# Optimization experiments

Measured on AMD Instinct MI355X. Metric: run time of the kernel, lower is better.

Reference implementation:

```python
import jax, jax.numpy as jnp
import numpy as np

SEQ = 2048
HID = 1024
NH = 16
HD = HID // NH


def setup_inputs() -> dict:
    key = jax.random.key(0)
    ks = jax.random.split(key, 5)
    s = 0.02
    return {
        "hidden_states": jax.random.normal(ks[0], (SEQ, HID), dtype=jnp.float32),
        "w_attn": jax.random.normal(ks[1], (HID, 3 * HID), dtype=jnp.float32) * s,
        "b_attn": jax.random.normal(ks[2], (3 * HID,), dtype=jnp.float32) * s,
        "w_proj": jax.random.normal(ks[3], (HID, HID), dtype=jnp.float32) * s,
        "b_proj": jax.random.normal(ks[4], (HID,), dtype=jnp.float32) * s,
    }


def reference(hidden_states, w_attn, b_attn, w_proj, b_proj):
    S = hidden_states.shape[0]
    qkv = hidden_states @ w_attn + b_attn          # [S, 3H]
    q, k, v = jnp.split(qkv, 3, axis=-1)
    q = q.reshape(S, NH, HD)
    k = k.reshape(S, NH, HD)
    v = v.reshape(S, NH, HD)
    sm_scale = 1.0 / np.sqrt(HD).astype(np.float32)
    # explicit scores [h, q, k] in fp32, as in the torch module
    scores = jnp.einsum('qhd,khd->hqk', q.astype(jnp.float32), k.astype(jnp.float32))
    scores = scores * sm_scale
    causal = jnp.tril(jnp.ones((S, S), dtype=bool))  # [q, k]
    scores = jnp.where(causal[None, :, :], scores, -jnp.inf)
    probs = jax.nn.softmax(scores, axis=-1)
    attn = jnp.einsum('hqk,khd->qhd', probs, v.astype(jnp.float32))  # [S, NH, HD]
    attn = attn.reshape(S, HID).astype(hidden_states.dtype)
    return attn @ w_proj + b_proj
```

## Files before the change

### kernel.cpp

```cpp
#include <hip/hip_runtime.h>
#include <cstdint>
#include <cstddef>

#define SEQ 2048
#define HID 1024
#define NHEAD 16
#define HDIM 64

typedef _Float16 f16;
typedef f16 half8 __attribute__((ext_vector_type(8)));
typedef f16 half4 __attribute__((ext_vector_type(4)));
typedef f16 half2_ __attribute__((ext_vector_type(2)));
typedef float f32x4 __attribute__((ext_vector_type(4)));

#define ASYNC_COPY16(g, l)                                                    \
  __builtin_amdgcn_global_load_lds(                                           \
      (const __attribute__((address_space(1))) void*)(const void*)(g),        \
      (__attribute__((address_space(3))) void*)(void*)(l), 16, 0, 0)

__global__ __launch_bounds__(256) void prologue(
    const float* __restrict__ h, const float* __restrict__ wa,
    const float* __restrict__ wp, f16* __restrict__ h16,
    f16* __restrict__ waT, f16* __restrict__ wpT) {
  const int b = blockIdx.x, tid = threadIdx.x;
  if (b >= 4096) {
    int i = ((b - 4096) * 256 + tid) * 4;
    float4 v = *(const float4*)(h + i);
    half4 o;
    o[0] = (f16)v.x; o[1] = (f16)v.y; o[2] = (f16)v.z; o[3] = (f16)v.w;
    *(half4*)(h16 + i) = o;
    return;
  }
  const float* src; f16* dst; int C, bx, by;
  if (b < 3072) { src = wa; dst = waT; C = 3072; bx = b % 96; by = b / 96; }
  else { int t = b - 3072; src = wp; dst = wpT; C = 1024; bx = t & 31; by = t >> 5; }
  __shared__ float tile[32][33];
  const int tx = tid & 31, ty = tid >> 5;
  const int c0 = bx * 32, r0 = by * 32;
#pragma unroll
  for (int i = 0; i < 32; i += 8)
    tile[ty + i][tx] = src[(size_t)(r0 + ty + i) * C + c0 + tx];
  __syncthreads();
#pragma unroll
  for (int i = 0; i < 32; i += 8)
    dst[(size_t)(c0 + ty + i) * 1024 + r0 + tx] = (f16)tile[tx][ty + i];
}

template <int BM, int BN, bool OUT16>
__global__ __launch_bounds__(256) void gemm_f16(
    const f16* __restrict__ A, const f16* __restrict__ Bt,
    const float* __restrict__ bias, void* __restrict__ Cout, int M, int N,
    int K) {
  constexpr int FM = BM / 32, FN = BN / 32;
  __shared__ __align__(16) f16 sA[BM * 32];
  __shared__ __align__(16) f16 sB[BN * 32];
  const int tid = threadIdx.x;
  const int wave = tid >> 6, lane = tid & 63;
  const int quad = lane >> 4, l16 = lane & 15;
  const int m0 = blockIdx.y * BM, n0 = blockIdx.x * BN;
  const int wm = (wave >> 1) * (BM / 2), wn = (wave & 1) * (BN / 2);
  const int rowA = lane >> 2, chunkA = lane & 3;

  f32x4 acc[FM][FN] = {};

  for (int k0 = 0; k0 < K; k0 += 32) {
#pragma unroll
    for (int r = wave; r < BM / 16; r += 4)
      ASYNC_COPY16(A + (size_t)(m0 + r * 16 + rowA) * K + k0 + chunkA * 8,
                   &sA[r * 512]);
#pragma unroll
    for (int r = wave; r < BN / 16; r += 4)
      ASYNC_COPY16(Bt + (size_t)(n0 + r * 16 + rowA) * K + k0 + chunkA * 8,
                   &sB[r * 512]);
    __syncthreads();

    half8 af[FM], bf[FN];
#pragma unroll
    for (int i = 0; i < FM; i++)
      af[i] = *(const half8*)&sA[(wm + i * 16 + l16) * 32 + quad * 8];
#pragma unroll
    for (int j = 0; j < FN; j++)
      bf[j] = *(const half8*)&sB[(wn + j * 16 + l16) * 32 + quad * 8];
#pragma unroll
    for (int i = 0; i < FM; i++)
#pragma unroll
      for (int j = 0; j < FN; j++)
        acc[i][j] = __builtin_amdgcn_mfma_f32_16x16x32_f16(af[i], bf[j],
                                                           acc[i][j], 0, 0, 0);
    __syncthreads();
  }

#pragma unroll
  for (int i = 0; i < FM; i++) {
    int row = m0 + wm + i * 16 + quad * 4;
#pragma unroll
    for (int j = 0; j < FN; j++) {
      int col = n0 + wn + j * 16 + l16;
      float bv = bias[col];
#pragma unroll
      for (int r = 0; r < 4; r++) {
        float v = acc[i][j][r] + bv;
        if (OUT16)
          ((f16*)Cout)[(size_t)(row + r) * N + col] = (f16)v;
        else
          ((float*)Cout)[(size_t)(row + r) * N + col] = v;
      }
    }
  }
}

#define LROW 72
__global__ __launch_bounds__(256, 3) void attn_split(
    const f16* __restrict__ qkv, f16* __restrict__ out,
    f16* __restrict__ Opart, float* __restrict__ ml) {
  const int b = blockIdx.x;
  const int h = b / 40;
  const int t = b % 40;
  int m, c, nc;
  if (t < 4)       { m = t;                 c = 0;      nc = 1; }
  else if (t < 12) { int u = t - 4;  m = 4 + (u >> 1);  c = u & 1; nc = 2; }
  else if (t < 24) { int u = t - 12; m = 8 + u / 3;     c = u % 3; nc = 3; }
  else             { int u = t - 24; m = 12 + (u >> 2); c = u & 3; nc = 4; }
  const int q0 = m * 128;
  const int T = 2 * m + 2;
  const int kt0 = c * 8;
  const int kt1 = (kt0 + 8 < T) ? kt0 + 8 : T;
  const int maskFrom = 2 * m;

  __shared__ __align__(16) f16 sK[64 * LROW];
  __shared__ __align__(16) f16 sVt[64 * LROW];
  __shared__ __align__(16) f16 sP[4][32 * LROW];

  const int tid = threadIdx.x;
  const int wave = tid >> 6, lane = tid & 63;
  const int quad = lane >> 4, l16 = lane & 15;

  const f16 qs = (f16)0.18033688f;
  half8 qf[2][2];
#pragma unroll
  for (int g = 0; g < 2; g++) {
    const f16* qb = qkv + (size_t)(q0 + wave * 32 + g * 16 + l16) * 3072 +
                    h * HDIM + quad * 8;
    qf[g][0] = *(const half8*)qb;
    qf[g][1] = *(const half8*)(qb + 32);
#pragma unroll
    for (int j = 0; j < 8; j++) { qf[g][0][j] *= qs; qf[g][1][j] *= qs; }
  }

  const f16* kbase = qkv + HID + h * HDIM;
  const f16* vbase = qkv + 2 * HID + h * HDIM;
  const int ks_row = tid >> 3, ks_cc = tid & 7;
  const int vs_d = tid & 63, vs_g = tid >> 6;

  f32x4 o[2][4] = {};
  float m_i[2] = {-1e30f, -1e30f}, l_i[2] = {0.f, 0.f};
  half8 kreg[2], vreg[2];

  auto prefetch = [&](int kt) {
    const int k0 = kt * 64;
#pragma unroll
    for (int i = 0; i < 2; i++) {
      kreg[i] = *(const half8*)(kbase + (size_t)(k0 + ks_row + i * 32) * 3072 +
                                ks_cc * 8);
      half8 col;
#pragma unroll
      for (int j = 0; j < 8; j++)
        col[j] = vbase[(size_t)(k0 + (vs_g + i * 4) * 8 + j) * 3072 + vs_d];
      vreg[i] = col;
    }
  };

  prefetch(kt0);
  for (int kt = kt0; kt < kt1; kt++) {
    const int k0 = kt * 64;
#pragma unroll
    for (int i = 0; i < 2; i++) {
      *(half8*)&sK[(ks_row + i * 32) * LROW + ks_cc * 8] = kreg[i];
      *(half8*)&sVt[vs_d * LROW + (vs_g + i * 4) * 8] = vreg[i];
    }
    __syncthreads();
    if (kt + 1 < kt1) prefetch(kt + 1);

    f32x4 sacc[2][4] = {};
#pragma unroll
    for (int kb = 0; kb < 4; kb++) {
      half8 kf0 = *(const half8*)&sK[(kb * 16 + l16) * LROW + quad * 8];
      half8 kf1 = *(const half8*)&sK[(kb * 16 + l16) * LROW + 32 + quad * 8];
#pragma unroll
      for (int g = 0; g < 2; g++) {
        sacc[g][kb] = __builtin_amdgcn_mfma_f32_16x16x32_f16(kf0, qf[g][0],
                                                             sacc[g][kb], 0, 0, 0);
        sacc[g][kb] = __builtin_amdgcn_mfma_f32_16x16x32_f16(kf1, qf[g][1],
                                                             sacc[g][kb], 0, 0, 0);
      }
    }
    if (kt >= maskFrom) {
#pragma unroll
      for (int g = 0; g < 2; g++) {
        const int qg = q0 + wave * 32 + g * 16 + l16;
#pragma unroll
        for (int kb = 0; kb < 4; kb++) {
          int kg = k0 + kb * 16 + quad * 4;
#pragma unroll
          for (int r = 0; r < 4; r++)
            if (kg + r > qg) sacc[g][kb][r] = -1e30f;
        }
      }
    }
#pragma unroll
    for (int g = 0; g < 2; g++) {
      float mx = -1e30f;
#pragma unroll
      for (int kb = 0; kb < 4; kb++)
#pragma unroll
        for (int r = 0; r < 4; r++) mx = fmaxf(mx, sacc[g][kb][r]);
      mx = fmaxf(mx, __shfl_xor(mx, 16));
      mx = fmaxf(mx, __shfl_xor(mx, 32));
      const float mnew = fmaxf(m_i[g], mx);
      const float alpha = exp2f(m_i[g] - mnew);
      float rs = 0.f;
#pragma unroll
      for (int kb = 0; kb < 4; kb++)
#pragma unroll
        for (int r = 0; r < 4; r++) {
          float p = exp2f(sacc[g][kb][r] - mnew);
          sacc[g][kb][r] = p;
          rs += p;
        }
      rs += __shfl_xor(rs, 16);
      rs += __shfl_xor(rs, 32);
      l_i[g] = l_i[g] * alpha + rs;
      m_i[g] = mnew;
#pragma unroll
      for (int j = 0; j < 4; j++)
#pragma unroll
        for (int r = 0; r < 4; r++) o[g][j][r] *= alpha;
      f16* pw = &sP[wave][(g * 16 + l16) * LROW];
#pragma unroll
      for (int kb = 0; kb < 4; kb++)
#pragma unroll
        for (int rp = 0; rp < 2; rp++) {
          half2_ pv;
          pv[0] = (f16)sacc[g][kb][rp * 2];
          pv[1] = (f16)sacc[g][kb][rp * 2 + 1];
          *(half2_*)&pw[kb * 16 + quad * 4 + rp * 2] = pv;
        }
    }
#pragma unroll
    for (int j = 0; j < 4; j++) {
      half8 vf0 = *(const half8*)&sVt[(j * 16 + l16) * LROW + quad * 8];
      half8 vf1 = *(const half8*)&sVt[(j * 16 + l16) * LROW + 32 + quad * 8];
#pragma unroll
      for (int g = 0; g < 2; g++) {
        half8 pf0 = *(const half8*)&sP[wave][(g * 16 + l16) * LROW + quad * 8];
        half8 pf1 =
            *(const half8*)&sP[wave][(g * 16 + l16) * LROW + 32 + quad * 8];
        o[g][j] = __builtin_amdgcn_mfma_f32_16x16x32_f16(vf0, pf0, o[g][j], 0, 0, 0);
        o[g][j] = __builtin_amdgcn_mfma_f32_16x16x32_f16(vf1, pf1, o[g][j], 0, 0, 0);
      }
    }
    __syncthreads();
  }

  if (nc == 1) {
#pragma unroll
    for (int g = 0; g < 2; g++) {
      const float inv = 1.f / l_i[g];
      f16* orow =
          out + (size_t)(q0 + wave * 32 + g * 16 + l16) * HID + h * HDIM;
#pragma unroll
      for (int j = 0; j < 4; j++) {
        half4 hv;
#pragma unroll
        for (int r = 0; r < 4; r++) hv[r] = (f16)(o[g][j][r] * inv);
        *(half4*)&orow[j * 16 + quad * 4] = hv;
      }
    }
  } else {
    int base;
    if (m < 8)       base = (m - 4) * 2;
    else if (m < 12) base = 8 + (m - 8) * 3;
    else             base = 20 + (m - 12) * 4;
    const int slot = h * 36 + base + c;
#pragma unroll
    for (int g = 0; g < 2; g++) {
      const int qrow = wave * 32 + g * 16 + l16;
      f16* op = Opart + (size_t)slot * 8192 + qrow * 64;
#pragma unroll
      for (int j = 0; j < 4; j++) {
        half4 hv;
#pragma unroll
        for (int r = 0; r < 4; r++) hv[r] = (f16)o[g][j][r];
        *(half4*)&op[j * 16 + quad * 4] = hv;
      }
      if (quad == 0) {
        ml[slot * 256 + qrow] = m_i[g];
        ml[slot * 256 + 128 + qrow] = l_i[g];
      }
    }
  }
}

__global__ __launch_bounds__(256) void attn_combine(
    const f16* __restrict__ Opart, const float* __restrict__ ml,
    f16* __restrict__ out) {
  int idx = blockIdx.x * 256 + threadIdx.x;
  int d = idx & 63;
  int row = (idx >> 6) & 127;
  int rest = idx >> 13;
  int mi = rest % 12;
  int h = rest / 12;
  int m = 4 + mi;
  int nc = (mi < 4) ? 2 : (mi < 8) ? 3 : 4;
  int base = (mi < 4) ? mi * 2 : (mi < 8) ? 8 + (mi - 4) * 3 : 20 + (mi - 8) * 4;
  int slot0 = h * 36 + base;

  float mm[4], ll[4];
  float M = -1e30f;
  for (int cc = 0; cc < nc; cc++) {
    mm[cc] = ml[(slot0 + cc) * 256 + row];
    ll[cc] = ml[(slot0 + cc) * 256 + 128 + row];
    M = fmaxf(M, mm[cc]);
  }
  float L = 0.f, acc = 0.f;
  for (int cc = 0; cc < nc; cc++) {
    float w = exp2f(mm[cc] - M);
    L += w * ll[cc];
    acc += w * (float)Opart[(size_t)(slot0 + cc) * 8192 + row * 64 + d];
  }
  out[(size_t)(m * 128 + row) * HID + h * HDIM + d] = (f16)(acc / L);
}

extern "C" void kernel_launch(void* const* d_in, const int* in_sizes, int n_in,
                              void* d_out, int out_size, void* d_ws,
                              size_t ws_size, hipStream_t stream) {
  const float* h = (const float*)d_in[0];
  const float* wa = (const float*)d_in[1];
  const float* ba = (const float*)d_in[2];
  const float* wp = (const float*)d_in[3];
  const float* bp = (const float*)d_in[4];
  float* out = (float*)d_out;

  char* ws = (char*)d_ws;
  f16* h16 = (f16*)(ws);
  f16* waT = (f16*)(ws + (4u << 20));
  f16* wpT = (f16*)(ws + (10u << 20));
  f16* qkv = (f16*)(ws + (12u << 20));
  f16* attn = (f16*)(ws + (24u << 20));
  f16* Opart = (f16*)(ws);
  float* mlbuf = (float*)(ws + 9437184);

  prologue<<<6144, 256, 0, stream>>>(h, wa, wp, h16, waT, wpT);
  gemm_f16<128, 128, true><<<dim3(24, 16), 256, 0, stream>>>(
      h16, waT, ba, qkv, SEQ, 3 * HID, HID);
  attn_split<<<640, 256, 0, stream>>>(qkv, attn, Opart, mlbuf);
  attn_combine<<<6144, 256, 0, stream>>>(Opart, mlbuf, attn);
  gemm_f16<64, 64, false><<<dim3(16, 32), 256, 0, stream>>>(
      attn, wpT, bp, out, SEQ, HID, HID);
}
```

Measured before the change: 160.5 us.

## Fuse input conversion into QKV GEMM, pre-transpose V, load attention tiles from global

The separate fp32-to-fp16 pass over hidden states is removed. The QKV GEMM now reads fp32 A directly and converts it while storing to LDS. A new kernel transposes V per head into a contiguous buffer, and the attention kernel drops its LDS staging of K and V, register prefetch and block barriers, reading MFMA fragments straight from global memory (mostly L2). This trades LDS traffic and syncs for more redundant global loads across waves and one extra launch. The launch-bounds occupancy hint on the attention kernel is also relaxed.

```diff
diff --git a/kernel.cpp b/kernel.cpp
--- a/kernel.cpp
+++ b/kernel.cpp
@@ -19,18 +19,9 @@
       (__attribute__((address_space(3))) void*)(void*)(l), 16, 0, 0)
 
 __global__ __launch_bounds__(256) void prologue(
-    const float* __restrict__ h, const float* __restrict__ wa,
-    const float* __restrict__ wp, f16* __restrict__ h16,
+    const float* __restrict__ wa, const float* __restrict__ wp,
     f16* __restrict__ waT, f16* __restrict__ wpT) {
   const int b = blockIdx.x, tid = threadIdx.x;
-  if (b >= 4096) {
-    int i = ((b - 4096) * 256 + tid) * 4;
-    float4 v = *(const float4*)(h + i);
-    half4 o;
-    o[0] = (f16)v.x; o[1] = (f16)v.y; o[2] = (f16)v.z; o[3] = (f16)v.w;
-    *(half4*)(h16 + i) = o;
-    return;
-  }
   const float* src; f16* dst; int C, bx, by;
   if (b < 3072) { src = wa; dst = waT; C = 3072; bx = b % 96; by = b / 96; }
   else { int t = b - 3072; src = wp; dst = wpT; C = 1024; bx = t & 31; by = t >> 5; }
@@ -46,9 +37,27 @@
     dst[(size_t)(c0 + ty + i) * 1024 + r0 + tx] = (f16)tile[tx][ty + i];
 }
 
-template <int BM, int BN, bool OUT16>
+__global__ __launch_bounds__(256) void vtrans(const f16* __restrict__ qkv,
+                                              f16* __restrict__ Vt) {
+  const int b = blockIdx.x, tid = threadIdx.x;
+  const int h = b >> 7, t = b & 127;
+  const int s0 = (t >> 1) * 32, d0 = (t & 1) * 32;
+  __shared__ f16 tile[32][33];
+  const int tx = tid & 31, ty = tid >> 5;
+#pragma unroll
+  for (int i = 0; i < 32; i += 8)
+    tile[ty + i][tx] =
+        qkv[(size_t)(s0 + ty + i) * 3072 + 2 * HID + h * HDIM + d0 + tx];
+  __syncthreads();
+#pragma unroll
+  for (int i = 0; i < 32; i += 8)
+    Vt[(size_t)h * HDIM * SEQ + (size_t)(d0 + ty + i) * SEQ + s0 + tx] =
+        tile[tx][ty + i];
+}
+
+template <int BM, int BN, bool OUT16, bool AF32>
 __global__ __launch_bounds__(256) void gemm_f16(
-    const f16* __restrict__ A, const f16* __restrict__ Bt,
+    const void* __restrict__ Ap, const f16* __restrict__ Bt,
     const float* __restrict__ bias, void* __restrict__ Cout, int M, int N,
     int K) {
   constexpr int FM = BM / 32, FN = BN / 32;
@@ -64,10 +73,25 @@
   f32x4 acc[FM][FN] = {};
 
   for (int k0 = 0; k0 < K; k0 += 32) {
-#pragma unroll
-    for (int r = wave; r < BM / 16; r += 4)
-      ASYNC_COPY16(A + (size_t)(m0 + r * 16 + rowA) * K + k0 + chunkA * 8,
-                   &sA[r * 512]);
+    if (AF32) {
+      const int row = tid >> 1, kh = (tid & 1) * 16;
+      const float* p = (const float*)Ap + (size_t)(m0 + row) * K + k0 + kh;
+      float4 a0 = ((const float4*)p)[0], a1 = ((const float4*)p)[1];
+      float4 a2 = ((const float4*)p)[2], a3 = ((const float4*)p)[3];
+      half8 h0, h1;
+      h0[0] = (f16)a0.x; h0[1] = (f16)a0.y; h0[2] = (f16)a0.z; h0[3] = (f16)a0.w;
+      h0[4] = (f16)a1.x; h0[5] = (f16)a1.y; h0[6] = (f16)a1.z; h0[7] = (f16)a1.w;
+      h1[0] = (f16)a2.x; h1[1] = (f16)a2.y; h1[2] = (f16)a2.z; h1[3] = (f16)a2.w;
+      h1[4] = (f16)a3.x; h1[5] = (f16)a3.y; h1[6] = (f16)a3.z; h1[7] = (f16)a3.w;
+      *(half8*)&sA[row * 32 + kh] = h0;
+      *(half8*)&sA[row * 32 + kh + 8] = h1;
+    } else {
+      const f16* A = (const f16*)Ap;
+#pragma unroll
+      for (int r = wave; r < BM / 16; r += 4)
+        ASYNC_COPY16(A + (size_t)(m0 + r * 16 + rowA) * K + k0 + chunkA * 8,
+                     &sA[r * 512]);
+    }
 #pragma unroll
     for (int r = wave; r < BN / 16; r += 4)
       ASYNC_COPY16(Bt + (size_t)(n0 + r * 16 + rowA) * K + k0 + chunkA * 8,
@@ -110,9 +134,9 @@
 }
 
 #define LROW 72
-__global__ __launch_bounds__(256, 3) void attn_split(
-    const f16* __restrict__ qkv, f16* __restrict__ out,
-    f16* __restrict__ Opart, float* __restrict__ ml) {
+__global__ __launch_bounds__(256) void attn_split(
+    const f16* __restrict__ qkv, const f16* __restrict__ Vt,
+    f16* __restrict__ out, f16* __restrict__ Opart, float* __restrict__ ml) {
   const int b = blockIdx.x;
   const int h = b / 40;
   const int t = b % 40;
@@ -127,8 +151,6 @@
   const int kt1 = (kt0 + 8 < T) ? kt0 + 8 : T;
   const int maskFrom = 2 * m;
 
-  __shared__ __align__(16) f16 sK[64 * LROW];
-  __shared__ __align__(16) f16 sVt[64 * LROW];
   __shared__ __align__(16) f16 sP[4][32 * LROW];
 
   const int tid = threadIdx.x;
@@ -148,44 +170,20 @@
   }
 
   const f16* kbase = qkv + HID + h * HDIM;
-  const f16* vbase = qkv + 2 * HID + h * HDIM;
-  const int ks_row = tid >> 3, ks_cc = tid & 7;
-  const int vs_d = tid & 63, vs_g = tid >> 6;
+  const f16* vtb = Vt + (size_t)h * HDIM * SEQ;
 
   f32x4 o[2][4] = {};
   float m_i[2] = {-1e30f, -1e30f}, l_i[2] = {0.f, 0.f};
-  half8 kreg[2], vreg[2];
-
-  auto prefetch = [&](int kt) {
-    const int k0 = kt * 64;
-#pragma unroll
-    for (int i = 0; i < 2; i++) {
-      kreg[i] = *(const half8*)(kbase + (size_t)(k0 + ks_row + i * 32) * 3072 +
-                                ks_cc * 8);
-      half8 col;
-#pragma unroll
-      for (int j = 0; j < 8; j++)
-        col[j] = vbase[(size_t)(k0 + (vs_g + i * 4) * 8 + j) * 3072 + vs_d];
-      vreg[i] = col;
-    }
-  };
-
-  prefetch(kt0);
+
   for (int kt = kt0; kt < kt1; kt++) {
     const int k0 = kt * 64;
-#pragma unroll
-    for (int i = 0; i < 2; i++) {
-      *(half8*)&sK[(ks_row + i * 32) * LROW + ks_cc * 8] = kreg[i];
-      *(half8*)&sVt[vs_d * LROW + (vs_g + i * 4) * 8] = vreg[i];
-    }
-    __syncthreads();
-    if (kt + 1 < kt1) prefetch(kt + 1);
 
     f32x4 sacc[2][4] = {};
 #pragma unroll
     for (int kb = 0; kb < 4; kb++) {
-      half8 kf0 = *(const half8*)&sK[(kb * 16 + l16) * LROW + quad * 8];
-      half8 kf1 = *(const half8*)&sK[(kb * 16 + l16) * LROW + 32 + quad * 8];
+      const f16* kp = kbase + (size_t)(k0 + kb * 16 + l16) * 3072 + quad * 8;
+      half8 kf0 = *(const half8*)kp;
+      half8 kf1 = *(const half8*)(kp + 32);
 #pragma unroll
       for (int g = 0; g < 2; g++) {
         sacc[g][kb] = __builtin_amdgcn_mfma_f32_16x16x32_f16(kf0, qf[g][0],
@@ -193,6 +191,13 @@
         sacc[g][kb] = __builtin_amdgcn_mfma_f32_16x16x32_f16(kf1, qf[g][1],
                                                              sacc[g][kb], 0, 0, 0);
       }
+    }
+    half8 vf[4][2];
+#pragma unroll
+    for (int j = 0; j < 4; j++) {
+      const f16* vp = vtb + (size_t)(j * 16 + l16) * SEQ + k0 + quad * 8;
+      vf[j][0] = *(const half8*)vp;
+      vf[j][1] = *(const half8*)(vp + 32);
     }
     if (kt >= maskFrom) {
 #pragma unroll
@@ -248,18 +253,17 @@
     }
 #pragma unroll
     for (int j = 0; j < 4; j++) {
-      half8 vf0 = *(const half8*)&sVt[(j * 16 + l16) * LROW + quad * 8];
-      half8 vf1 = *(const half8*)&sVt[(j * 16 + l16) * LROW + 32 + quad * 8];
 #pragma unroll
       for (int g = 0; g < 2; g++) {
         half8 pf0 = *(const half8*)&sP[wave][(g * 16 + l16) * LROW + quad * 8];
         half8 pf1 =
             *(const half8*)&sP[wave][(g * 16 + l16) * LROW + 32 + quad * 8];
-        o[g][j] = __builtin_amdgcn_mfma_f32_16x16x32_f16(vf0, pf0, o[g][j], 0, 0, 0);
-        o[g][j] = __builtin_amdgcn_mfma_f32_16x16x32_f16(vf1, pf1, o[g][j], 0, 0, 0);
-      }
-    }
-    __syncthreads();
+        o[g][j] = __builtin_amdgcn_mfma_f32_16x16x32_f16(vf[j][0], pf0,
+                                                         o[g][j], 0, 0, 0);
+        o[g][j] = __builtin_amdgcn_mfma_f32_16x16x32_f16(vf[j][1], pf1,
+                                                         o[g][j], 0, 0, 0);
+      }
+    }
   }
 
   if (nc == 1) {
@@ -342,19 +346,20 @@
   float* out = (float*)d_out;
 
   char* ws = (char*)d_ws;
-  f16* h16 = (f16*)(ws);
-  f16* waT = (f16*)(ws + (4u << 20));
-  f16* wpT = (f16*)(ws + (10u << 20));
-  f16* qkv = (f16*)(ws + (12u << 20));
+  f16* waT = (f16*)(ws);
+  f16* wpT = (f16*)(ws + (6u << 20));
+  f16* qkv = (f16*)(ws + (8u << 20));
+  f16* Vt = (f16*)(ws + (20u << 20));
   f16* attn = (f16*)(ws + (24u << 20));
-  f16* Opart = (f16*)(ws);
-  float* mlbuf = (float*)(ws + 9437184);
-
-  prologue<<<6144, 256, 0, stream>>>(h, wa, wp, h16, waT, wpT);
-  gemm_f16<128, 128, true><<<dim3(24, 16), 256, 0, stream>>>(
-      h16, waT, ba, qkv, SEQ, 3 * HID, HID);
-  attn_split<<<640, 256, 0, stream>>>(qkv, attn, Opart, mlbuf);
+  f16* Opart = (f16*)(ws + (28u << 20));
+  float* mlbuf = (float*)(ws + (28u << 20) + 9437184);
+
+  prologue<<<4096, 256, 0, stream>>>(wa, wp, waT, wpT);
+  gemm_f16<128, 128, true, true><<<dim3(24, 16), 256, 0, stream>>>(
+      h, waT, ba, qkv, SEQ, 3 * HID, HID);
+  vtrans<<<2048, 256, 0, stream>>>(qkv, Vt);
+  attn_split<<<640, 256, 0, stream>>>(qkv, Vt, attn, Opart, mlbuf);
   attn_combine<<<6144, 256, 0, stream>>>(Opart, mlbuf, attn);
-  gemm_f16<64, 64, false><<<dim3(16, 32), 256, 0, stream>>>(
+  gemm_f16<64, 64, false, false><<<dim3(16, 32), 256, 0, stream>>>(
       attn, wpT, bp, out, SEQ, HID, HID);
 }
```

New measurement: 194.6 us. 1.21x slower.
